# Kernel tuning notes

Measured on AMD Instinct MI355X. Metric: run time of the kernel, lower is better.

## Reference

```python
import jax, jax.numpy as jnp
import numpy as np

TURBO_BLOCK_SIZE = 64
TURBO_MSE_BITS = 5
QMAX = 2 ** (TURBO_MSE_BITS - 1) - 1  # 15 for symmetric int5
# MSE scale search grid: shrink factors applied to the max-abs scale
SHRINKS = np.linspace(0.4, 1.0, 16)


def mse_quant_dequant(w):
    """Block-wise (block=64, along input dim) symmetric int5 quantize-dequantize.
    Per block, searches a grid of shrunken max-abs scales and keeps the one
    minimizing reconstruction MSE."""
    O, I = w.shape
    wb = w.reshape(O, I // TURBO_BLOCK_SIZE, TURBO_BLOCK_SIZE)
    amax = jnp.max(jnp.abs(wb), axis=-1, keepdims=True)
    base = jnp.maximum(amax, 1e-8) / QMAX
    best_err = jnp.full(amax.shape, jnp.inf, dtype=w.dtype)
    best_scale = base
    for s in SHRINKS:  # fixed small grid, not a data-dim loop
        scale = base * jnp.asarray(s, dtype=w.dtype)
        deq = jnp.clip(jnp.round(wb / scale), -QMAX, QMAX) * scale
        err = jnp.sum((deq - wb) ** 2, axis=-1, keepdims=True)
        upd = err < best_err
        best_err = jnp.where(upd, err, best_err)
        best_scale = jnp.where(upd, scale, best_scale)
    deq = jnp.clip(jnp.round(wb / best_scale), -QMAX, QMAX) * best_scale
    return deq.reshape(O, I)


def turbo_linear(x, w):
    # Straight-through estimator: forward uses quantized weights,
    # gradient flows to w as identity.
    wq = w + jax.lax.stop_gradient(mse_quant_dequant(w) - w)
    return x @ wq.T


def setup_inputs() -> dict:
    key = jax.random.key(0)
    k1, k2, k3 = jax.random.split(key, 3)
    dim, mlp_mult = 2048, 4
    hidden = mlp_mult * dim
    x = jax.random.normal(k1, (4, 2048, dim), dtype=jnp.float32)
    w_fc = jax.random.normal(k2, (hidden, dim), dtype=jnp.float32) * 0.02
    w_proj = jax.random.normal(k3, (dim, hidden), dtype=jnp.float32) * 0.02
    return {"x": x, "w_fc": w_fc, "w_proj": w_proj}


def reference(x, w_fc, w_proj):
    h = jnp.maximum(turbo_linear(x, w_fc), 0.0)  # relu
    return turbo_linear(h * h, w_proj)           # relu-square then proj
```

## Files before the change

### kernel.cpp

```cpp
#include <hip/hip_runtime.h>
#include <hip/hip_bf16.h>

typedef __attribute__((ext_vector_type(8))) __bf16 bf16x8;
typedef __attribute__((ext_vector_type(4))) float f32x4;

__device__ __forceinline__ void gload_lds16(const void* g, void* lds) {
    __builtin_amdgcn_global_load_lds(
        (const __attribute__((address_space(1))) void*)g,
        (__attribute__((address_space(3))) void*)lds, 16, 0, 0);
}

__global__ __launch_bounds__(256) void quant_bf16_kernel(
    const float* __restrict__ w, __hip_bfloat16* __restrict__ wq, int nblk)
{
#pragma clang fp contract(off)
    int b = blockIdx.x * 256 + threadIdx.x;
    if (b >= nblk) return;
    const float4* src = (const float4*)(w + (size_t)b * 64);
    float v[64];
#pragma unroll
    for (int i = 0; i < 16; ++i) {
        float4 t = src[i];
        v[i*4+0] = t.x; v[i*4+1] = t.y; v[i*4+2] = t.z; v[i*4+3] = t.w;
    }
    float amax = 0.0f;
#pragma unroll
    for (int i = 0; i < 64; ++i) amax = fmaxf(amax, fabsf(v[i]));
    float base = fmaxf(amax, 1e-8f) / 15.0f;

    float best_err = __builtin_inff();
    float best_scale = base, best_rs = 0.0f;
    for (int k = 0; k < 16; ++k) {
        double sd = (k == 15) ? 1.0 : ((double)k * (0.6 / 15.0) + 0.4);
        float scale = base * (float)sd;
        float rs = 1.0f / scale;
        float err = 0.0f;
#pragma unroll
        for (int i = 0; i < 64; ++i) {
            float q = rintf(v[i] * rs);
            q = fminf(fmaxf(q, -15.0f), 15.0f);
            float d = q * scale - v[i];
            err = err + d * d;
        }
        if (err < best_err) { best_err = err; best_scale = scale; best_rs = rs; }
    }
    __hip_bfloat16* dst = wq + (size_t)b * 64;
#pragma unroll
    for (int i = 0; i < 64; ++i) {
        float q = rintf(v[i] * best_rs);
        q = fminf(fmaxf(q, -15.0f), 15.0f);
        dst[i] = __float2bfloat16(q * best_scale);
    }
}

__global__ __launch_bounds__(256) void f32_to_bf16_kernel(
    const float* __restrict__ in, __hip_bfloat16* __restrict__ out, int n8)
{
    int i = blockIdx.x * 256 + threadIdx.x;
    if (i >= n8) return;
    const float4* p = (const float4*)(in + (size_t)i * 8);
    float4 a = p[0], b = p[1];
    alignas(16) __hip_bfloat16 r[8];
    r[0] = __float2bfloat16(a.x); r[1] = __float2bfloat16(a.y);
    r[2] = __float2bfloat16(a.z); r[3] = __float2bfloat16(a.w);
    r[4] = __float2bfloat16(b.x); r[5] = __float2bfloat16(b.y);
    r[6] = __float2bfloat16(b.z); r[7] = __float2bfloat16(b.w);
    *(uint4*)(out + (size_t)i * 8) = *(const uint4*)r;
}

#define LDA2(d, base, s) { \
    d[0] = *(const bf16x8*)(smem + (base) + aB + (s)*2048u + cb0); \
    d[1] = *(const bf16x8*)(smem + (base) + aB + (s)*2048u + cb1); }

#define LDB8(base) { \
    bf[0][0] = *(const bf16x8*)(smem + (base) + bB + 0u    + cb0); \
    bf[0][1] = *(const bf16x8*)(smem + (base) + bB + 0u    + cb1); \
    bf[1][0] = *(const bf16x8*)(smem + (base) + bB + 2048u + cb0); \
    bf[1][1] = *(const bf16x8*)(smem + (base) + bB + 2048u + cb1); \
    bf[2][0] = *(const bf16x8*)(smem + (base) + bB + 4096u + cb0); \
    bf[2][1] = *(const bf16x8*)(smem + (base) + bB + 4096u + cb1); \
    bf[3][0] = *(const bf16x8*)(smem + (base) + bB + 6144u + cb0); \
    bf[3][1] = *(const bf16x8*)(smem + (base) + bB + 6144u + cb1); }

#define MF8(q, a2) { \
    acc[q][0] = __builtin_amdgcn_mfma_f32_16x16x32_bf16(a2[0], bf[0][0], acc[q][0],0,0,0); \
    acc[q][0] = __builtin_amdgcn_mfma_f32_16x16x32_bf16(a2[1], bf[0][1], acc[q][0],0,0,0); \
    acc[q][1] = __builtin_amdgcn_mfma_f32_16x16x32_bf16(a2[0], bf[1][0], acc[q][1],0,0,0); \
    acc[q][1] = __builtin_amdgcn_mfma_f32_16x16x32_bf16(a2[1], bf[1][1], acc[q][1],0,0,0); \
    acc[q][2] = __builtin_amdgcn_mfma_f32_16x16x32_bf16(a2[0], bf[2][0], acc[q][2],0,0,0); \
    acc[q][2] = __builtin_amdgcn_mfma_f32_16x16x32_bf16(a2[1], bf[2][1], acc[q][2],0,0,0); \
    acc[q][3] = __builtin_amdgcn_mfma_f32_16x16x32_bf16(a2[0], bf[3][0], acc[q][3],0,0,0); \
    acc[q][3] = __builtin_amdgcn_mfma_f32_16x16x32_bf16(a2[1], bf[3][1], acc[q][3],0,0,0); }

#define STAGE(base, eoff, ldsOff) \
    gload_lds16((base) + (size_t)((eoff) + voff), smem + (ldsOff) + wOff)

#define SB0() __builtin_amdgcn_sched_barrier(0)
#define LGKM(n) { asm volatile("s_waitcnt lgkmcnt(" #n ")" ::: "memory"); SB0(); }
#define BARRIER() { SB0(); __builtin_amdgcn_s_barrier(); SB0(); }

template <int EPI>
__global__ __launch_bounds__(512, 1) void gemm256_kernel(
    const __hip_bfloat16* __restrict__ A,
    const __hip_bfloat16* __restrict__ B,
    void* __restrict__ Cout, int M, int N, int K)
{
    extern __shared__ char smem[];

    const int t    = threadIdx.x;
    const int lane = t & 63;
    const int w    = t >> 6;
    const int wr   = w >> 2;
    const int wc   = w & 3;
    const int lo   = lane & 15;
    const int hi   = lane >> 4;
    const uint wOff = (uint)w * 1024u;

    const int cpx = gridDim.x >> 3;
    int bid = blockIdx.x;
    bid = (bid & 7) * cpx + (bid >> 3);
    const int nN = N >> 8;
    const int bm = bid / nN;
    const int bn = bid % nN;
    const int rowBase = bm << 8;
    const int colBase = bn << 8;

    const __hip_bfloat16* uA = A + (size_t)rowBase * (size_t)K;
    const __hip_bfloat16* uB = B + (size_t)colBase * (size_t)K;
    uint o0 = (uint)t * 16u;
    uint p0 = o0 ^ (((o0 >> 7) & 7u) << 4);
    const uint voff = (p0 >> 7) * (uint)K + ((p0 & 127u) >> 1);
    const uint K64 = (uint)K * 64u;

    const uint sw  = (uint)(lo & 7) << 4;
    const uint aB  = (uint)wr * 16384u + (uint)lo * 128u;
    const uint bB  = 32768u + (uint)(wc >> 1) * 16384u
                   + ((uint)(wc & 1) * 64u + (uint)lo) * 128u;
    const uint cb0 = ((uint)hi * 16u) ^ sw;
    const uint cb1 = (64u + (uint)hi * 16u) ^ sw;

    f32x4 acc[8][4] = {};
    bf16x8 aC0[2], aC1[2], aD0[2], aD1[2], bf[4][2];

    STAGE(uA, 0u,     0u);      STAGE(uA, K64,    8192u);
    STAGE(uA, 2u*K64, 16384u);  STAGE(uA, 3u*K64, 24576u);
    STAGE(uB, 0u,     32768u);  STAGE(uB, K64,    40960u);
    STAGE(uB, 2u*K64, 49152u);  STAGE(uB, 3u*K64, 57344u);
    asm volatile("s_waitcnt vmcnt(0)" ::: "memory");
    BARRIER();

    const int NT = K >> 6;
    for (int tt = 0; tt < NT; ++tt) {
        const uint bufOff = (uint)(tt & 1) * 65536u;
        const uint nxtOff = bufOff ^ 65536u;
        const bool pf = (tt + 1 < NT);
        const uint kN = ((uint)(tt + 1)) << 6;

        if (pf) {
            STAGE(uA, kN,          nxtOff + 0u);
            STAGE(uA, kN + K64,    nxtOff + 8192u);
            STAGE(uA, kN + 2u*K64, nxtOff + 16384u);
            STAGE(uA, kN + 3u*K64, nxtOff + 24576u);
            STAGE(uB, kN,          nxtOff + 32768u);
            STAGE(uB, kN + K64,    nxtOff + 40960u);
            STAGE(uB, kN + 2u*K64, nxtOff + 49152u);
            STAGE(uB, kN + 3u*K64, nxtOff + 57344u);
        }
        SB0();

        LDB8(bufOff);
        LDA2(aC0, bufOff, 0u); LDA2(aC1, bufOff, 1u);
        SB0();
        LDA2(aD0, bufOff, 2u); LDA2(aD1, bufOff, 3u);

        LGKM(4);
        __builtin_amdgcn_s_setprio(1); MF8(0, aC0); MF8(1, aC1); __builtin_amdgcn_s_setprio(0);
        LDA2(aC0, bufOff, 4u); LDA2(aC1, bufOff, 5u);

        LGKM(4);
        __builtin_amdgcn_s_setprio(1); MF8(2, aD0); MF8(3, aD1); __builtin_amdgcn_s_setprio(0);
        LDA2(aD0, bufOff, 6u); LDA2(aD1, bufOff, 7u);

        LGKM(4);
        __builtin_amdgcn_s_setprio(1); MF8(4, aC0); MF8(5, aC1); __builtin_amdgcn_s_setprio(0);

        LGKM(0);
        __builtin_amdgcn_s_setprio(1); MF8(6, aD0); MF8(7, aD1); __builtin_amdgcn_s_setprio(0);

        if (pf) asm volatile("s_waitcnt vmcnt(0)" ::: "memory");
        BARRIER();
    }

    if (EPI == 0) {
        __hip_bfloat16* Cb = (__hip_bfloat16*)Cout;
#pragma unroll
        for (int i = 0; i < 8; ++i)
#pragma unroll
            for (int j = 0; j < 4; ++j)
#pragma unroll
                for (int r = 0; r < 4; ++r) {
                    size_t row = rowBase + wr*128 + i*16 + hi*4 + r;
                    size_t col = colBase + wc*64 + j*16 + lo;
                    float v = fmaxf(acc[i][j][r], 0.0f);
                    Cb[row * N + col] = __float2bfloat16(v * v);
                }
    } else {
        float* Cf = (float*)Cout;
#pragma unroll
        for (int i = 0; i < 8; ++i)
#pragma unroll
            for (int j = 0; j < 4; ++j)
#pragma unroll
                for (int r = 0; r < 4; ++r) {
                    size_t row = rowBase + wr*128 + i*16 + hi*4 + r;
                    size_t col = colBase + wc*64 + j*16 + lo;
                    Cf[row * N + col] = acc[i][j][r];
                }
    }
}

extern "C" void kernel_launch(void* const* d_in, const int* in_sizes, int n_in,
                              void* d_out, int out_size, void* d_ws, size_t ws_size,
                              hipStream_t stream) {
    const float* x      = (const float*)d_in[0];
    const float* w_fc   = (const float*)d_in[1];
    const float* w_proj = (const float*)d_in[2];
    float* out = (float*)d_out;

    const int DIM = 2048, HID = 8192, M = 8192;

    char* ws = (char*)d_ws;
    __hip_bfloat16* Xb  = (__hip_bfloat16*)ws;
    __hip_bfloat16* Wfc = (__hip_bfloat16*)(ws + (size_t)M * DIM * 2);
    __hip_bfloat16* Wpj = (__hip_bfloat16*)(ws + (size_t)(M * DIM + (size_t)HID * DIM) * 2);
    __hip_bfloat16* H2  = (__hip_bfloat16*)(ws + (size_t)(M * DIM + 2 * (size_t)HID * DIM) * 2);

    (void)hipFuncSetAttribute((const void*)gemm256_kernel<0>,
                              hipFuncAttributeMaxDynamicSharedMemorySize, 131072);
    (void)hipFuncSetAttribute((const void*)gemm256_kernel<1>,
                              hipFuncAttributeMaxDynamicSharedMemorySize, 131072);

    int nblk = HID * DIM / 64;
    quant_bf16_kernel<<<nblk / 256, 256, 0, stream>>>(w_fc, Wfc, nblk);
    quant_bf16_kernel<<<nblk / 256, 256, 0, stream>>>(w_proj, Wpj, nblk);

    int n8 = M * DIM / 8;
    f32_to_bf16_kernel<<<n8 / 256, 256, 0, stream>>>(x, Xb, n8);

    gemm256_kernel<0><<<(M/256)*(HID/256), 512, 131072, stream>>>(
        Xb, Wfc, (void*)H2, M, HID, DIM);

    gemm256_kernel<1><<<(M/256)*(DIM/256), 512, 131072, stream>>>(
        H2, Wpj, (void*)out, M, DIM, HID);
}
```

Before: 610.7 us.

## Shrink GEMM tile to 256x128 with K=32 steps and two blocks per CU

Result: slower. 657.3 us (+7.6%).

```diff
diff --git a/kernel.cpp b/kernel.cpp
--- a/kernel.cpp
+++ b/kernel.cpp
@@ -68,39 +68,13 @@
     *(uint4*)(out + (size_t)i * 8) = *(const uint4*)r;
 }
 
-#define LDA2(d, base, s) { \
-    d[0] = *(const bf16x8*)(smem + (base) + aB + (s)*2048u + cb0); \
-    d[1] = *(const bf16x8*)(smem + (base) + aB + (s)*2048u + cb1); }
-
-#define LDB8(base) { \
-    bf[0][0] = *(const bf16x8*)(smem + (base) + bB + 0u    + cb0); \
-    bf[0][1] = *(const bf16x8*)(smem + (base) + bB + 0u    + cb1); \
-    bf[1][0] = *(const bf16x8*)(smem + (base) + bB + 2048u + cb0); \
-    bf[1][1] = *(const bf16x8*)(smem + (base) + bB + 2048u + cb1); \
-    bf[2][0] = *(const bf16x8*)(smem + (base) + bB + 4096u + cb0); \
-    bf[2][1] = *(const bf16x8*)(smem + (base) + bB + 4096u + cb1); \
-    bf[3][0] = *(const bf16x8*)(smem + (base) + bB + 6144u + cb0); \
-    bf[3][1] = *(const bf16x8*)(smem + (base) + bB + 6144u + cb1); }
-
-#define MF8(q, a2) { \
-    acc[q][0] = __builtin_amdgcn_mfma_f32_16x16x32_bf16(a2[0], bf[0][0], acc[q][0],0,0,0); \
-    acc[q][0] = __builtin_amdgcn_mfma_f32_16x16x32_bf16(a2[1], bf[0][1], acc[q][0],0,0,0); \
-    acc[q][1] = __builtin_amdgcn_mfma_f32_16x16x32_bf16(a2[0], bf[1][0], acc[q][1],0,0,0); \
-    acc[q][1] = __builtin_amdgcn_mfma_f32_16x16x32_bf16(a2[1], bf[1][1], acc[q][1],0,0,0); \
-    acc[q][2] = __builtin_amdgcn_mfma_f32_16x16x32_bf16(a2[0], bf[2][0], acc[q][2],0,0,0); \
-    acc[q][2] = __builtin_amdgcn_mfma_f32_16x16x32_bf16(a2[1], bf[2][1], acc[q][2],0,0,0); \
-    acc[q][3] = __builtin_amdgcn_mfma_f32_16x16x32_bf16(a2[0], bf[3][0], acc[q][3],0,0,0); \
-    acc[q][3] = __builtin_amdgcn_mfma_f32_16x16x32_bf16(a2[1], bf[3][1], acc[q][3],0,0,0); }
-
+#define SB0() __builtin_amdgcn_sched_barrier(0)
+#define BARRIER() { SB0(); __builtin_amdgcn_s_barrier(); SB0(); }
 #define STAGE(base, eoff, ldsOff) \
     gload_lds16((base) + (size_t)((eoff) + voff), smem + (ldsOff) + wOff)
 
-#define SB0() __builtin_amdgcn_sched_barrier(0)
-#define LGKM(n) { asm volatile("s_waitcnt lgkmcnt(" #n ")" ::: "memory"); SB0(); }
-#define BARRIER() { SB0(); __builtin_amdgcn_s_barrier(); SB0(); }
-
 template <int EPI>
-__global__ __launch_bounds__(512, 1) void gemm256_kernel(
+__global__ __launch_bounds__(256, 2) void gemm256_kernel(
     const __hip_bfloat16* __restrict__ A,
     const __hip_bfloat16* __restrict__ B,
     void* __restrict__ Cout, int M, int N, int K)
@@ -110,8 +84,8 @@
     const int t    = threadIdx.x;
     const int lane = t & 63;
     const int w    = t >> 6;
-    const int wr   = w >> 2;
-    const int wc   = w & 3;
+    const int wr   = w >> 1;
+    const int wc   = w & 1;
     const int lo   = lane & 15;
     const int hi   = lane >> 4;
     const uint wOff = (uint)w * 1024u;
@@ -119,73 +93,65 @@
     const int cpx = gridDim.x >> 3;
     int bid = blockIdx.x;
     bid = (bid & 7) * cpx + (bid >> 3);
-    const int nN = N >> 8;
+    const int nN = N >> 7;
     const int bm = bid / nN;
     const int bn = bid % nN;
     const int rowBase = bm << 8;
-    const int colBase = bn << 8;
+    const int colBase = bn << 7;
 
     const __hip_bfloat16* uA = A + (size_t)rowBase * (size_t)K;
     const __hip_bfloat16* uB = B + (size_t)colBase * (size_t)K;
-    uint o0 = (uint)t * 16u;
-    uint p0 = o0 ^ (((o0 >> 7) & 7u) << 4);
-    const uint voff = (p0 >> 7) * (uint)K + ((p0 & 127u) >> 1);
+
+    const uint voff = ((uint)(t >> 2)) * (uint)K
+                    + ((((uint)t & 3u) ^ (((uint)t >> 3) & 3u)) * 8u);
     const uint K64 = (uint)K * 64u;
 
-    const uint sw  = (uint)(lo & 7) << 4;
-    const uint aB  = (uint)wr * 16384u + (uint)lo * 128u;
-    const uint bB  = 32768u + (uint)(wc >> 1) * 16384u
-                   + ((uint)(wc & 1) * 64u + (uint)lo) * 128u;
-    const uint cb0 = ((uint)hi * 16u) ^ sw;
-    const uint cb1 = (64u + (uint)hi * 16u) ^ sw;
+    const uint laneOff = (uint)lo * 64u
+                       + ((((uint)hi) ^ (((uint)lo >> 1) & 3u)) << 4);
+    const uint aFB = (uint)wr * 8192u + laneOff;
+    const uint bFB = 16384u + (uint)wc * 4096u + laneOff;
 
     f32x4 acc[8][4] = {};
-    bf16x8 aC0[2], aC1[2], aD0[2], aD1[2], bf[4][2];
-
-    STAGE(uA, 0u,     0u);      STAGE(uA, K64,    8192u);
-    STAGE(uA, 2u*K64, 16384u);  STAGE(uA, 3u*K64, 24576u);
-    STAGE(uB, 0u,     32768u);  STAGE(uB, K64,    40960u);
-    STAGE(uB, 2u*K64, 49152u);  STAGE(uB, 3u*K64, 57344u);
+
+    STAGE(uA, 0u,     0u);      STAGE(uA, K64,    4096u);
+    STAGE(uA, 2u*K64, 8192u);   STAGE(uA, 3u*K64, 12288u);
+    STAGE(uB, 0u,     16384u);  STAGE(uB, K64,    20480u);
     asm volatile("s_waitcnt vmcnt(0)" ::: "memory");
     BARRIER();
 
-    const int NT = K >> 6;
+    const int NT = K >> 5;
     for (int tt = 0; tt < NT; ++tt) {
-        const uint bufOff = (uint)(tt & 1) * 65536u;
-        const uint nxtOff = bufOff ^ 65536u;
+        const uint bufOff = (uint)(tt & 1) * 24576u;
+        const uint nxtOff = bufOff ^ 24576u;
         const bool pf = (tt + 1 < NT);
-        const uint kN = ((uint)(tt + 1)) << 6;
+        const uint kN = ((uint)(tt + 1)) << 5;
 
         if (pf) {
             STAGE(uA, kN,          nxtOff + 0u);
-            STAGE(uA, kN + K64,    nxtOff + 8192u);
-            STAGE(uA, kN + 2u*K64, nxtOff + 16384u);
-            STAGE(uA, kN + 3u*K64, nxtOff + 24576u);
-            STAGE(uB, kN,          nxtOff + 32768u);
-            STAGE(uB, kN + K64,    nxtOff + 40960u);
-            STAGE(uB, kN + 2u*K64, nxtOff + 49152u);
-            STAGE(uB, kN + 3u*K64, nxtOff + 57344u);
+            STAGE(uA, kN + K64,    nxtOff + 4096u);
+            STAGE(uA, kN + 2u*K64, nxtOff + 8192u);
+            STAGE(uA, kN + 3u*K64, nxtOff + 12288u);
+            STAGE(uB, kN,          nxtOff + 16384u);
+            STAGE(uB, kN + K64,    nxtOff + 20480u);
         }
         SB0();
 
-        LDB8(bufOff);
-        LDA2(aC0, bufOff, 0u); LDA2(aC1, bufOff, 1u);
-        SB0();
-        LDA2(aD0, bufOff, 2u); LDA2(aD1, bufOff, 3u);
-
-        LGKM(4);
-        __builtin_amdgcn_s_setprio(1); MF8(0, aC0); MF8(1, aC1); __builtin_amdgcn_s_setprio(0);
-        LDA2(aC0, bufOff, 4u); LDA2(aC1, bufOff, 5u);
-
-        LGKM(4);
-        __builtin_amdgcn_s_setprio(1); MF8(2, aD0); MF8(3, aD1); __builtin_amdgcn_s_setprio(0);
-        LDA2(aD0, bufOff, 6u); LDA2(aD1, bufOff, 7u);
-
-        LGKM(4);
-        __builtin_amdgcn_s_setprio(1); MF8(4, aC0); MF8(5, aC1); __builtin_amdgcn_s_setprio(0);
-
-        LGKM(0);
-        __builtin_amdgcn_s_setprio(1); MF8(6, aD0); MF8(7, aD1); __builtin_amdgcn_s_setprio(0);
+        bf16x8 bfr[4], afr[8];
+#pragma unroll
+        for (int j = 0; j < 4; ++j)
+            bfr[j] = *(const bf16x8*)(smem + bufOff + bFB + (uint)j * 1024u);
+#pragma unroll
+        for (int i = 0; i < 8; ++i)
+            afr[i] = *(const bf16x8*)(smem + bufOff + aFB + (uint)i * 1024u);
+
+        __builtin_amdgcn_s_setprio(1);
+#pragma unroll
+        for (int i = 0; i < 8; ++i)
+#pragma unroll
+            for (int j = 0; j < 4; ++j)
+                acc[i][j] = __builtin_amdgcn_mfma_f32_16x16x32_bf16(
+                    afr[i], bfr[j], acc[i][j], 0, 0, 0);
+        __builtin_amdgcn_s_setprio(0);
 
         if (pf) asm volatile("s_waitcnt vmcnt(0)" ::: "memory");
         BARRIER();
@@ -236,9 +202,9 @@
     __hip_bfloat16* H2  = (__hip_bfloat16*)(ws + (size_t)(M * DIM + 2 * (size_t)HID * DIM) * 2);
 
     (void)hipFuncSetAttribute((const void*)gemm256_kernel<0>,
-                              hipFuncAttributeMaxDynamicSharedMemorySize, 131072);
+                              hipFuncAttributeMaxDynamicSharedMemorySize, 49152);
     (void)hipFuncSetAttribute((const void*)gemm256_kernel<1>,
-                              hipFuncAttributeMaxDynamicSharedMemorySize, 131072);
+                              hipFuncAttributeMaxDynamicSharedMemorySize, 49152);
 
     int nblk = HID * DIM / 64;
     quant_bf16_kernel<<<nblk / 256, 256, 0, stream>>>(w_fc, Wfc, nblk);
@@ -247,9 +213,9 @@
     int n8 = M * DIM / 8;
     f32_to_bf16_kernel<<<n8 / 256, 256, 0, stream>>>(x, Xb, n8);
 
-    gemm256_kernel<0><<<(M/256)*(HID/256), 512, 131072, stream>>>(
+    gemm256_kernel<0><<<(M/256)*(HID/128), 256, 49152, stream>>>(
         Xb, Wfc, (void*)H2, M, HID, DIM);
 
-    gemm256_kernel<1><<<(M/256)*(DIM/256), 512, 131072, stream>>>(
+    gemm256_kernel<1><<<(M/256)*(DIM/128), 256, 49152, stream>>>(
         H2, Wpj, (void*)out, M, DIM, HID);
 }
```

## Load B fragments directly from global into registers, stage only A in LDS

Applied to the files above, without the earlier changes.

Measured after the change: 829.8 us. 35.9% more time.

```diff
diff --git a/kernel.cpp b/kernel.cpp
--- a/kernel.cpp
+++ b/kernel.cpp
@@ -72,32 +72,59 @@
     d[0] = *(const bf16x8*)(smem + (base) + aB + (s)*2048u + cb0); \
     d[1] = *(const bf16x8*)(smem + (base) + aB + (s)*2048u + cb1); }
 
-#define LDB8(base) { \
-    bf[0][0] = *(const bf16x8*)(smem + (base) + bB + 0u    + cb0); \
-    bf[0][1] = *(const bf16x8*)(smem + (base) + bB + 0u    + cb1); \
-    bf[1][0] = *(const bf16x8*)(smem + (base) + bB + 2048u + cb0); \
-    bf[1][1] = *(const bf16x8*)(smem + (base) + bB + 2048u + cb1); \
-    bf[2][0] = *(const bf16x8*)(smem + (base) + bB + 4096u + cb0); \
-    bf[2][1] = *(const bf16x8*)(smem + (base) + bB + 4096u + cb1); \
-    bf[3][0] = *(const bf16x8*)(smem + (base) + bB + 6144u + cb0); \
-    bf[3][1] = *(const bf16x8*)(smem + (base) + bB + 6144u + cb1); }
-
-#define MF8(q, a2) { \
-    acc[q][0] = __builtin_amdgcn_mfma_f32_16x16x32_bf16(a2[0], bf[0][0], acc[q][0],0,0,0); \
-    acc[q][0] = __builtin_amdgcn_mfma_f32_16x16x32_bf16(a2[1], bf[0][1], acc[q][0],0,0,0); \
-    acc[q][1] = __builtin_amdgcn_mfma_f32_16x16x32_bf16(a2[0], bf[1][0], acc[q][1],0,0,0); \
-    acc[q][1] = __builtin_amdgcn_mfma_f32_16x16x32_bf16(a2[1], bf[1][1], acc[q][1],0,0,0); \
-    acc[q][2] = __builtin_amdgcn_mfma_f32_16x16x32_bf16(a2[0], bf[2][0], acc[q][2],0,0,0); \
-    acc[q][2] = __builtin_amdgcn_mfma_f32_16x16x32_bf16(a2[1], bf[2][1], acc[q][2],0,0,0); \
-    acc[q][3] = __builtin_amdgcn_mfma_f32_16x16x32_bf16(a2[0], bf[3][0], acc[q][3],0,0,0); \
-    acc[q][3] = __builtin_amdgcn_mfma_f32_16x16x32_bf16(a2[1], bf[3][1], acc[q][3],0,0,0); }
-
-#define STAGE(base, eoff, ldsOff) \
-    gload_lds16((base) + (size_t)((eoff) + voff), smem + (ldsOff) + wOff)
+#define BLOAD(dst, kk) { \
+    dst[0][0] = *(const bf16x8*)(uB + (size_t)(rB + 0u*K16 + (kk))); \
+    dst[0][1] = *(const bf16x8*)(uB + (size_t)(rB + 0u*K16 + 32u + (kk))); \
+    dst[1][0] = *(const bf16x8*)(uB + (size_t)(rB + 1u*K16 + (kk))); \
+    dst[1][1] = *(const bf16x8*)(uB + (size_t)(rB + 1u*K16 + 32u + (kk))); \
+    dst[2][0] = *(const bf16x8*)(uB + (size_t)(rB + 2u*K16 + (kk))); \
+    dst[2][1] = *(const bf16x8*)(uB + (size_t)(rB + 2u*K16 + 32u + (kk))); \
+    dst[3][0] = *(const bf16x8*)(uB + (size_t)(rB + 3u*K16 + (kk))); \
+    dst[3][1] = *(const bf16x8*)(uB + (size_t)(rB + 3u*K16 + 32u + (kk))); }
+
+#define MF8(q, a2, B) { \
+    acc[q][0] = __builtin_amdgcn_mfma_f32_16x16x32_bf16(a2[0], B[0][0], acc[q][0],0,0,0); \
+    acc[q][0] = __builtin_amdgcn_mfma_f32_16x16x32_bf16(a2[1], B[0][1], acc[q][0],0,0,0); \
+    acc[q][1] = __builtin_amdgcn_mfma_f32_16x16x32_bf16(a2[0], B[1][0], acc[q][1],0,0,0); \
+    acc[q][1] = __builtin_amdgcn_mfma_f32_16x16x32_bf16(a2[1], B[1][1], acc[q][1],0,0,0); \
+    acc[q][2] = __builtin_amdgcn_mfma_f32_16x16x32_bf16(a2[0], B[2][0], acc[q][2],0,0,0); \
+    acc[q][2] = __builtin_amdgcn_mfma_f32_16x16x32_bf16(a2[1], B[2][1], acc[q][2],0,0,0); \
+    acc[q][3] = __builtin_amdgcn_mfma_f32_16x16x32_bf16(a2[0], B[3][0], acc[q][3],0,0,0); \
+    acc[q][3] = __builtin_amdgcn_mfma_f32_16x16x32_bf16(a2[1], B[3][1], acc[q][3],0,0,0); }
+
+#define STAGEA(eoff, ldsOff) \
+    gload_lds16(uA + (size_t)((eoff) + voff), smem + (ldsOff) + wOff)
 
 #define SB0() __builtin_amdgcn_sched_barrier(0)
-#define LGKM(n) { asm volatile("s_waitcnt lgkmcnt(" #n ")" ::: "memory"); SB0(); }
 #define BARRIER() { SB0(); __builtin_amdgcn_s_barrier(); SB0(); }
+
+#define TILE_BODY(bufOff, nxtOff, bCur, bNxt, kNxt, PF) { \
+    if (PF) { \
+        STAGEA((kNxt),          (nxtOff) + 0u); \
+        STAGEA((kNxt) + K64,    (nxtOff) + 8192u); \
+        STAGEA((kNxt) + 2u*K64, (nxtOff) + 16384u); \
+        STAGEA((kNxt) + 3u*K64, (nxtOff) + 24576u); \
+        BLOAD(bNxt, (kNxt)); \
+    } \
+    SB0(); \
+    LDA2(aC0, (bufOff), 0u); LDA2(aC1, (bufOff), 1u); \
+    __builtin_amdgcn_s_setprio(1); \
+    MF8(0, aC0, bCur); LDA2(aC0, (bufOff), 2u); \
+    MF8(1, aC1, bCur); LDA2(aC1, (bufOff), 3u); \
+    __builtin_amdgcn_s_setprio(0); \
+    __builtin_amdgcn_s_setprio(1); \
+    MF8(2, aC0, bCur); LDA2(aC0, (bufOff), 4u); \
+    MF8(3, aC1, bCur); LDA2(aC1, (bufOff), 5u); \
+    __builtin_amdgcn_s_setprio(0); \
+    __builtin_amdgcn_s_setprio(1); \
+    MF8(4, aC0, bCur); LDA2(aC0, (bufOff), 6u); \
+    MF8(5, aC1, bCur); LDA2(aC1, (bufOff), 7u); \
+    __builtin_amdgcn_s_setprio(0); \
+    __builtin_amdgcn_s_setprio(1); \
+    MF8(6, aC0, bCur); MF8(7, aC1, bCur); \
+    __builtin_amdgcn_s_setprio(0); \
+    if (PF) asm volatile("s_waitcnt vmcnt(0)" ::: "memory"); \
+    BARRIER(); }
 
 template <int EPI>
 __global__ __launch_bounds__(512, 1) void gemm256_kernel(
@@ -127,68 +154,36 @@
 
     const __hip_bfloat16* uA = A + (size_t)rowBase * (size_t)K;
     const __hip_bfloat16* uB = B + (size_t)colBase * (size_t)K;
+
     uint o0 = (uint)t * 16u;
     uint p0 = o0 ^ (((o0 >> 7) & 7u) << 4);
     const uint voff = (p0 >> 7) * (uint)K + ((p0 & 127u) >> 1);
     const uint K64 = (uint)K * 64u;
+    const uint K16 = (uint)K * 16u;
+
+    const uint rB = ((uint)(wc * 64 + lo)) * (uint)K + (uint)hi * 8u;
 
     const uint sw  = (uint)(lo & 7) << 4;
     const uint aB  = (uint)wr * 16384u + (uint)lo * 128u;
-    const uint bB  = 32768u + (uint)(wc >> 1) * 16384u
-                   + ((uint)(wc & 1) * 64u + (uint)lo) * 128u;
     const uint cb0 = ((uint)hi * 16u) ^ sw;
     const uint cb1 = (64u + (uint)hi * 16u) ^ sw;
 
     f32x4 acc[8][4] = {};
-    bf16x8 aC0[2], aC1[2], aD0[2], aD1[2], bf[4][2];
-
-    STAGE(uA, 0u,     0u);      STAGE(uA, K64,    8192u);
-    STAGE(uA, 2u*K64, 16384u);  STAGE(uA, 3u*K64, 24576u);
-    STAGE(uB, 0u,     32768u);  STAGE(uB, K64,    40960u);
-    STAGE(uB, 2u*K64, 49152u);  STAGE(uB, 3u*K64, 57344u);
+    bf16x8 aC0[2], aC1[2], bE[4][2], bO[4][2];
+
+    STAGEA(0u,     0u);      STAGEA(K64,    8192u);
+    STAGEA(2u*K64, 16384u);  STAGEA(3u*K64, 24576u);
+    BLOAD(bE, 0u);
     asm volatile("s_waitcnt vmcnt(0)" ::: "memory");
     BARRIER();
 
-    const int NT = K >> 6;
-    for (int tt = 0; tt < NT; ++tt) {
-        const uint bufOff = (uint)(tt & 1) * 65536u;
-        const uint nxtOff = bufOff ^ 65536u;
-        const bool pf = (tt + 1 < NT);
-        const uint kN = ((uint)(tt + 1)) << 6;
-
-        if (pf) {
-            STAGE(uA, kN,          nxtOff + 0u);
-            STAGE(uA, kN + K64,    nxtOff + 8192u);
-            STAGE(uA, kN + 2u*K64, nxtOff + 16384u);
-            STAGE(uA, kN + 3u*K64, nxtOff + 24576u);
-            STAGE(uB, kN,          nxtOff + 32768u);
-            STAGE(uB, kN + K64,    nxtOff + 40960u);
-            STAGE(uB, kN + 2u*K64, nxtOff + 49152u);
-            STAGE(uB, kN + 3u*K64, nxtOff + 57344u);
-        }
-        SB0();
-
-        LDB8(bufOff);
-        LDA2(aC0, bufOff, 0u); LDA2(aC1, bufOff, 1u);
-        SB0();
-        LDA2(aD0, bufOff, 2u); LDA2(aD1, bufOff, 3u);
-
-        LGKM(4);
-        __builtin_amdgcn_s_setprio(1); MF8(0, aC0); MF8(1, aC1); __builtin_amdgcn_s_setprio(0);
-        LDA2(aC0, bufOff, 4u); LDA2(aC1, bufOff, 5u);
-
-        LGKM(4);
-        __builtin_amdgcn_s_setprio(1); MF8(2, aD0); MF8(3, aD1); __builtin_amdgcn_s_setprio(0);
-        LDA2(aD0, bufOff, 6u); LDA2(aD1, bufOff, 7u);
-
-        LGKM(4);
-        __builtin_amdgcn_s_setprio(1); MF8(4, aC0); MF8(5, aC1); __builtin_amdgcn_s_setprio(0);
-
-        LGKM(0);
-        __builtin_amdgcn_s_setprio(1); MF8(6, aD0); MF8(7, aD1); __builtin_amdgcn_s_setprio(0);
-
-        if (pf) asm volatile("s_waitcnt vmcnt(0)" ::: "memory");
-        BARRIER();
+    const int NI = K >> 7;
+    for (int P = 0; P < NI; ++P) {
+        const uint kOdd  = ((uint)(2 * P + 1)) << 6;
+        const uint kEven = kOdd + 64u;
+        const bool pf2 = (P + 1 < NI);
+        TILE_BODY(0u,     32768u, bE, bO, kOdd,  true);
+        TILE_BODY(32768u, 0u,     bO, bE, kEven, pf2);
     }
 
     if (EPI == 0) {
@@ -236,9 +231,9 @@
     __hip_bfloat16* H2  = (__hip_bfloat16*)(ws + (size_t)(M * DIM + 2 * (size_t)HID * DIM) * 2);
 
     (void)hipFuncSetAttribute((const void*)gemm256_kernel<0>,
-                              hipFuncAttributeMaxDynamicSharedMemorySize, 131072);
+                              hipFuncAttributeMaxDynamicSharedMemorySize, 65536);
     (void)hipFuncSetAttribute((const void*)gemm256_kernel<1>,
-                              hipFuncAttributeMaxDynamicSharedMemorySize, 131072);
+                              hipFuncAttributeMaxDynamicSharedMemorySize, 65536);
 
     int nblk = HID * DIM / 64;
     quant_bf16_kernel<<<nblk / 256, 256, 0, stream>>>(w_fc, Wfc, nblk);
@@ -247,9 +242,9 @@
     int n8 = M * DIM / 8;
     f32_to_bf16_kernel<<<n8 / 256, 256, 0, stream>>>(x, Xb, n8);
 
-    gemm256_kernel<0><<<(M/256)*(HID/256), 512, 131072, stream>>>(
+    gemm256_kernel<0><<<(M/256)*(HID/256), 512, 65536, stream>>>(
         Xb, Wfc, (void*)H2, M, HID, DIM);
 
-    gemm256_kernel<1><<<(M/256)*(DIM/256), 512, 131072, stream>>>(
+    gemm256_kernel<1><<<(M/256)*(DIM/256), 512, 65536, stream>>>(
         H2, Wpj, (void*)out, M, DIM, HID);
 }
```
